# Kernel tuning notes

Hardware: AMD Instinct MI355X
Metric: run time of the kernel (lower is better)

Reference implementation:

```python
import jax, jax.numpy as jnp
import numpy as np

B, T, C, H = 4, 2048, 1024, 16
D = C // H  # head dim = 64


def setup_inputs() -> dict:
    key = jax.random.key(0)
    ks = jax.random.split(key, 5)
    s = 1.0 / np.sqrt(C)
    return {
        "x": jax.random.normal(ks[0], (B, T, C), jnp.float32),
        "Wq": jax.random.normal(ks[1], (C, C), jnp.float32) * s,
        "bq": jnp.zeros((C,), jnp.float32),
        "Wk": jax.random.normal(ks[2], (C, C), jnp.float32) * s,
        "bk": jnp.zeros((C,), jnp.float32),
        "Wv": jax.random.normal(ks[3], (C, C), jnp.float32) * s,
        "bv": jnp.zeros((C,), jnp.float32),
        "Wp": jax.random.normal(ks[4], (C, C), jnp.float32) * s,
        "bp": jnp.zeros((C,), jnp.float32),
    }


def reference(x, Wq, bq, Wk, bk, Wv, bv, Wp, bp):
    # linear projections -> [B, H, T, D]
    def heads(t):
        return t.reshape(B, T, H, D).transpose(0, 2, 1, 3)
    q = heads(x @ Wq.T + bq)
    k = heads(x @ Wk.T + bk)
    v = heads(x @ Wv.T + bv)
    scale = 1.0 / np.sqrt(D)
    att = jnp.einsum("bhtd,bhsd->bhts", q, k) * scale  # [B,H,T,T]
    causal = jnp.tril(jnp.ones((T, T), bool))
    att = jnp.where(causal[None, None], att, -jnp.inf)
    att = jax.nn.softmax(att, axis=-1)
    y = jnp.einsum("bhts,bhsd->bhtd", att, v)  # [B,H,T,D]
    y = y.transpose(0, 2, 1, 3).reshape(B, T, C)
    return y @ Wp.T + bp
```

## Files before the change

### kernel.cpp

```cpp
#include <hip/hip_runtime.h>

typedef float f32x4 __attribute__((ext_vector_type(4)));
typedef float f32x16 __attribute__((ext_vector_type(16)));
typedef __bf16 bf16x8 __attribute__((ext_vector_type(8)));
typedef unsigned short u16x8 __attribute__((ext_vector_type(8)));

#define SCQ 0.1803368801111183f

__device__ inline unsigned short f2bf(float f) {
  unsigned int u = __builtin_bit_cast(unsigned int, f);
  u += 0x7FFFu + ((u >> 16) & 1u);
  return (unsigned short)(u >> 16);
}
__device__ inline unsigned short f2bf_fast(float f) {
  unsigned int u = __builtin_bit_cast(unsigned int, f);
  return (unsigned short)((u + 0x8000u) >> 16);
}

__device__ inline float fexp2(float x) {
#if __has_builtin(__builtin_amdgcn_exp2f)
  return __builtin_amdgcn_exp2f(x);
#else
  return exp2f(x);
#endif
}

template <int N>
__device__ inline float rowror(float v) {
  return __builtin_bit_cast(float, __builtin_amdgcn_update_dpp(
      0, __builtin_bit_cast(int, v), 0x120 | N, 0xF, 0xF, true));
}
__device__ inline float rowsum16(float v) {
  v += rowror<8>(v); v += rowror<4>(v);
  v += rowror<2>(v); v += rowror<1>(v);
  return v;
}

__device__ inline void gload_lds16(const unsigned short* g, unsigned short* l) {
  __builtin_amdgcn_global_load_lds(
      (const __attribute__((address_space(1))) unsigned int*)g,
      (__attribute__((address_space(3))) unsigned int*)l, 16, 0, 0);
}

__global__ void cvt_x(const float* __restrict__ in, unsigned short* __restrict__ out) {
  int i = (blockIdx.x * 256 + threadIdx.x) * 4;
  float4 f = *(const float4*)(in + i);
  ushort4 o;
  o.x = f2bf(f.x); o.y = f2bf(f.y); o.z = f2bf(f.z); o.w = f2bf(f.w);
  *(ushort4*)(out + i) = o;
}

__global__ void cvt_w(const float* __restrict__ a, const float* __restrict__ b,
                      const float* __restrict__ c, const float* __restrict__ d,
                      unsigned short* __restrict__ oa, unsigned short* __restrict__ ob,
                      unsigned short* __restrict__ oc, unsigned short* __restrict__ od) {
  const float* src[4] = {a, b, c, d};
  unsigned short* dst[4] = {oa, ob, oc, od};
  int m = blockIdx.y;
  int i = (blockIdx.x * 256 + threadIdx.x) * 4;
  float4 f = *(const float4*)(src[m] + i);
  ushort4 o;
  o.x = f2bf(f.x); o.y = f2bf(f.y); o.z = f2bf(f.z); o.w = f2bf(f.w);
  *(ushort4*)(dst[m] + i) = o;
}

template <int MODE>
__global__ __launch_bounds__(256) void gemm128(const unsigned short* __restrict__ A,
                                               const unsigned short* __restrict__ Bt,
                                               const float* __restrict__ b0,
                                               const float* __restrict__ b1,
                                               const float* __restrict__ b2,
                                               void* __restrict__ out,
                                               int M, int N, int K) {
  __shared__ __align__(16) unsigned short As[128 * 64];
  __shared__ __align__(16) unsigned short Bs[128 * 64];
  const int tid = threadIdx.x;
  const int lane = tid & 63, w = tid >> 6;
  const int l31 = lane & 31, half = lane >> 5;
  const int wm = w & 1, wn = w >> 1;
  const int m0 = blockIdx.x * 128, n0 = blockIdx.y * 128;

  f32x16 acc[2][2] = {};

  for (int kb = 0; kb < K; kb += 64) {
#pragma unroll
    for (int j = 0; j < 4; j++) {
      int ch = j * 256 + w * 64 + lane;
      int row = ch >> 3, pc = ch & 7;
      int c = pc ^ (row & 7);
      gload_lds16(A + (size_t)(m0 + row) * K + kb + c * 8, As + (size_t)(j * 256 + w * 64) * 8);
      gload_lds16(Bt + (size_t)(n0 + row) * K + kb + c * 8, Bs + (size_t)(j * 256 + w * 64) * 8);
    }
    __syncthreads();
#pragma unroll
    for (int ks = 0; ks < 64; ks += 16) {
      bf16x8 af[2], bfr[2];
#pragma unroll
      for (int at = 0; at < 2; at++) {
        int row = wm * 64 + at * 32 + l31;
        int pc = ((ks >> 3) + half) ^ (row & 7);
        af[at] = *(const bf16x8*)(As + row * 64 + pc * 8);
      }
#pragma unroll
      for (int nt = 0; nt < 2; nt++) {
        int row = wn * 64 + nt * 32 + l31;
        int pc = ((ks >> 3) + half) ^ (row & 7);
        bfr[nt] = *(const bf16x8*)(Bs + row * 64 + pc * 8);
      }
#pragma unroll
      for (int at = 0; at < 2; at++)
#pragma unroll
        for (int nt = 0; nt < 2; nt++)
          acc[at][nt] = __builtin_amdgcn_mfma_f32_32x32x16_bf16(af[at], bfr[nt], acc[at][nt], 0, 0, 0);
    }
    __syncthreads();
  }

#pragma unroll
  for (int at = 0; at < 2; at++)
#pragma unroll
    for (int nt = 0; nt < 2; nt++) {
      int col = n0 + wn * 64 + nt * 32 + l31;
      float bv, sc;
      int which = 0, cl = col;
      if (MODE == 0) {
        which = col >> 10; cl = col & 1023;
        const float* bp = (which == 0) ? b0 : ((which == 1) ? b1 : b2);
        bv = bp[cl];
        sc = (which == 0) ? SCQ : 1.f;
      } else {
        bv = b0[col]; sc = 1.f;
      }
#pragma unroll
      for (int reg = 0; reg < 16; reg++) {
        int row = m0 + wm * 64 + at * 32 + (reg & 3) + 8 * (reg >> 2) + 4 * half;
        float v = (acc[at][nt][reg] + bv) * sc;
        if (MODE == 0) {
          int h = cl >> 6, d = cl & 63;
          int b = row >> 11, t = row & 2047;
          ((unsigned short*)out)[(size_t)which * 8388608 +
                                 ((size_t)((b * 16 + h) * 2048 + t)) * 64 + d] = f2bf(v);
        } else {
          ((float*)out)[(size_t)row * N + col] = v;
        }
      }
    }
}

__global__ __launch_bounds__(256) void transpose_v(const unsigned short* __restrict__ V,
                                                   unsigned short* __restrict__ Vt) {
  constexpr int P = 66;
  __shared__ unsigned short L[64 * P];
  const int tid = threadIdx.x;
  const int bh = blockIdx.y;
  const int t0 = blockIdx.x * 64;
  const unsigned short* Vp = V + (size_t)bh * 2048 * 64;
  unsigned short* Op = Vt + (size_t)bh * 64 * 2048;
#pragma unroll
  for (int j = 0; j < 2; j++) {
    int r = (tid >> 3) + j * 32;
    int c = (tid & 7) * 8;
    u16x8 v = *(const u16x8*)(Vp + (size_t)(t0 + r) * 64 + c);
#pragma unroll
    for (int i = 0; i < 4; i++) {
      unsigned int pk = (unsigned int)v[2 * i] | ((unsigned int)v[2 * i + 1] << 16);
      *(unsigned int*)&L[r * P + c + 2 * i] = pk;
    }
  }
  __syncthreads();
#pragma unroll
  for (int j = 0; j < 2; j++) {
    int ch = j * 256 + tid;
    int d = ch >> 3, tc = (ch & 7) * 8;
    u16x8 o;
#pragma unroll
    for (int k = 0; k < 8; k++) o[k] = L[(tc + k) * P + d];
    *(u16x8*)(Op + (size_t)d * 2048 + t0 + tc) = o;
  }
}

#define PPITCH 72
__device__ __attribute__((always_inline)) inline
void attn_tile(int qt, int s0, const bf16x8* aq, const unsigned short* Ks,
               const unsigned short* Vs, unsigned short* pl,
               f32x4* o, float* lrow, int quad, int l15) {
  const bool full = (s0 + 63) <= qt;
  const int nsc = full ? 4 : (((qt + 15 - s0) >> 4) + 1);
  const int nsc2 = (nsc + 1) & ~1;

#pragma unroll
  for (int sc = 0; sc < 4; sc++) {
    if (sc < nsc) {
      f32x4 s = {};
#pragma unroll
      for (int kh = 0; kh < 2; kh++) {
        int kr = sc * 16 + l15;
        int pc = (kh * 4 + quad) ^ (kr & 7);
        u16x8 bku = *(const u16x8*)(Ks + kr * 64 + pc * 8);
        s = __builtin_amdgcn_mfma_f32_16x16x32_bf16(aq[kh], __builtin_bit_cast(bf16x8, bku), s, 0, 0, 0);
      }
      if (full) {
#pragma unroll
        for (int r = 0; r < 4; r++) {
          float e = fexp2(s[r]);
          lrow[r] += e;
          pl[(quad * 4 + r) * PPITCH + sc * 16 + l15] = f2bf_fast(e);
        }
      } else {
        int sg = s0 + sc * 16 + l15;
#pragma unroll
        for (int r = 0; r < 4; r++) {
          float e = fexp2(s[r]);
          e = (sg > qt + quad * 4 + r) ? 0.f : e;
          lrow[r] += e;
          pl[(quad * 4 + r) * PPITCH + sc * 16 + l15] = f2bf_fast(e);
        }
      }
    } else if (sc < nsc2) {
#pragma unroll
      for (int r = 0; r < 4; r++)
        pl[(quad * 4 + r) * PPITCH + sc * 16 + l15] = 0;
    }
  }
  __asm__ __volatile__("" ::: "memory");
#pragma unroll
  for (int h2 = 0; h2 < 2; h2++) {
    if (h2 * 2 < nsc2) {
      u16x8 apu = *(const u16x8*)(pl + l15 * PPITCH + h2 * 32 + quad * 8);
      bf16x8 ap = __builtin_bit_cast(bf16x8, apu);
#pragma unroll
      for (int dc = 0; dc < 4; dc++) {
        int vr = dc * 16 + l15;
        int pc = (h2 * 4 + quad) ^ (vr & 7);
        u16x8 vu = *(const u16x8*)(Vs + vr * 64 + pc * 8);
        o[dc] = __builtin_amdgcn_mfma_f32_16x16x32_bf16(ap, __builtin_bit_cast(bf16x8, vu), o[dc], 0, 0, 0);
      }
    }
  }
}

__global__ __launch_bounds__(256, 2) void attn_kernel(const unsigned short* __restrict__ Q,
                                                      const unsigned short* __restrict__ Km,
                                                      const unsigned short* __restrict__ Vt,
                                                      unsigned short* __restrict__ Y) {
  constexpr int T = 2048, D = 64;
  __shared__ __align__(16) unsigned short Ks[2][64 * 64];
  __shared__ __align__(16) unsigned short Vs[2][64 * 64];
  __shared__ __align__(16) unsigned short P_lds[4][16 * PPITCH];
  const int tid = threadIdx.x;
  const int lane = tid & 63, w = tid >> 6;
  const int quad = lane >> 4, l15 = lane & 15;
  const int bh = blockIdx.y;
  const int b = bh >> 4, h = bh & 15;
  const int p = blockIdx.x;
  const unsigned short* Qp = Q + (size_t)bh * T * D;
  const unsigned short* Kp = Km + (size_t)bh * T * D;
  const unsigned short* Vp = Vt + (size_t)bh * D * T;
  unsigned short* pl = P_lds[w];

  const int bch0 = (w * 2) * 64, bch1 = (w * 2 + 1) * 64;
  const int ch0 = bch0 + lane, ch1 = bch1 + lane;
  const int row0 = ch0 >> 3, c0 = (ch0 & 7) ^ (row0 & 7);
  const int row1 = ch1 >> 3, c1 = (ch1 & 7) ^ (row1 & 7);

  for (int phase = 0; phase < 2; ++phase) {
    int jlo, jhi;
    if (!phase) { jlo = 8 * p + w; jhi = jlo + 4; }
    else        { jhi = 127 - 8 * p - w; jlo = jhi - 4; }
    const int qlo = jlo * 16, qhi = jhi * 16;
    const int nit = phase ? (32 - 2 * p) : (2 * p + 2);

    bf16x8 aqlo[2], aqhi[2];
    aqlo[0] = *(const bf16x8*)(Qp + (size_t)(qlo + l15) * D + quad * 8);
    aqlo[1] = *(const bf16x8*)(Qp + (size_t)(qlo + l15) * D + 32 + quad * 8);
    aqhi[0] = *(const bf16x8*)(Qp + (size_t)(qhi + l15) * D + quad * 8);
    aqhi[1] = *(const bf16x8*)(Qp + (size_t)(qhi + l15) * D + 32 + quad * 8);

    f32x4 olo[4] = {}, ohi[4] = {};
    float llo[4] = {0.f, 0.f, 0.f, 0.f}, lhi[4] = {0.f, 0.f, 0.f, 0.f};

    gload_lds16(Kp + (size_t)row0 * 64 + c0 * 8, Ks[0] + (size_t)bch0 * 8);
    gload_lds16(Kp + (size_t)row1 * 64 + c1 * 8, Ks[0] + (size_t)bch1 * 8);
    gload_lds16(Vp + (size_t)row0 * T + c0 * 8, Vs[0] + (size_t)bch0 * 8);
    gload_lds16(Vp + (size_t)row1 * T + c1 * 8, Vs[0] + (size_t)bch1 * 8);
    __syncthreads();

    for (int it = 0; it < nit; ++it) {
      const int s0 = it * 64;
      const int cur = it & 1, nxt = cur ^ 1;
      if (it + 1 < nit) {
        const int sn = s0 + 64;
        gload_lds16(Kp + (size_t)(sn + row0) * 64 + c0 * 8, Ks[nxt] + (size_t)bch0 * 8);
        gload_lds16(Kp + (size_t)(sn + row1) * 64 + c1 * 8, Ks[nxt] + (size_t)bch1 * 8);
        gload_lds16(Vp + (size_t)row0 * T + sn + c0 * 8, Vs[nxt] + (size_t)bch0 * 8);
        gload_lds16(Vp + (size_t)row1 * T + sn + c1 * 8, Vs[nxt] + (size_t)bch1 * 8);
      }
      if (s0 <= qlo + 15)
        attn_tile(qlo, s0, aqlo, Ks[cur], Vs[cur], pl, olo, llo, quad, l15);
      attn_tile(qhi, s0, aqhi, Ks[cur], Vs[cur], pl, ohi, lhi, quad, l15);
      __syncthreads();
    }

#pragma unroll
    for (int r = 0; r < 4; r++) {
      float ilo = 1.f / rowsum16(llo[r]);
      float ihi = 1.f / rowsum16(lhi[r]);
      int glo = qlo + quad * 4 + r, ghi = qhi + quad * 4 + r;
#pragma unroll
      for (int dc = 0; dc < 4; dc++) {
        Y[((size_t)(b * T + glo)) * 1024 + h * 64 + dc * 16 + l15] = f2bf(olo[dc][r] * ilo);
        Y[((size_t)(b * T + ghi)) * 1024 + h * 64 + dc * 16 + l15] = f2bf(ohi[dc][r] * ihi);
      }
    }
  }
}

extern "C" void kernel_launch(void* const* d_in, const int* in_sizes, int n_in,
                              void* d_out, int out_size, void* d_ws, size_t ws_size,
                              hipStream_t stream) {
  const float* x  = (const float*)d_in[0];
  const float* Wq = (const float*)d_in[1];
  const float* bq = (const float*)d_in[2];
  const float* Wk = (const float*)d_in[3];
  const float* bk = (const float*)d_in[4];
  const float* Wv = (const float*)d_in[5];
  const float* bv = (const float*)d_in[6];
  const float* Wp = (const float*)d_in[7];
  const float* bp = (const float*)d_in[8];

  char* ws = (char*)d_ws;
  unsigned short* xb  = (unsigned short*)(ws + 0);
  unsigned short* wqb = (unsigned short*)(ws + 16777216);
  unsigned short* wkb = (unsigned short*)(ws + 18874368);
  unsigned short* wvb = (unsigned short*)(ws + 20971520);
  unsigned short* wpb = (unsigned short*)(ws + 23068672);
  unsigned short* Qb  = (unsigned short*)(ws + 25165824);
  unsigned short* Kb  = (unsigned short*)(ws + 41943040);
  unsigned short* Vb  = (unsigned short*)(ws + 58720256);
  unsigned short* Vtb = xb;
  unsigned short* Yb  = Vb;

  cvt_x<<<8192, 256, 0, stream>>>(x, xb);
  cvt_w<<<dim3(1024, 4), 256, 0, stream>>>(Wq, Wk, Wv, Wp, wqb, wkb, wvb, wpb);

  gemm128<0><<<dim3(64, 24), 256, 0, stream>>>(xb, wqb, bq, bk, bv, Qb, 8192, 3072, 1024);

  transpose_v<<<dim3(32, 64), 256, 0, stream>>>(Vb, Vtb);
  attn_kernel<<<dim3(8, 64), 256, 0, stream>>>(Qb, Kb, Vtb, Yb);

  gemm128<1><<<dim3(64, 8), 256, 0, stream>>>(Yb, wpb, bp, bp, bp, d_out, 8192, 1024, 1024);
}
```

Before: 281.3 us.

## Split attention into more smaller blocks with single-buffered K/V and higher occupancy

The attention kernel now gives each wave one 16-row query tile per phase instead of two, and launches 1024 blocks instead of 512, with the grid reordered so consecutive blocks share a query-pair index across heads. K/V double buffering is removed to halve LDS, and launch bounds are raised to four blocks per SM to increase occupancy. Each block reloads K/V per tile and now synchronises twice per iteration with no prefetch overlap. Total K/V traffic also rises, because each K/V tile is now shared by four query tiles instead of eight.

```diff
diff --git a/kernel.cpp b/kernel.cpp
--- a/kernel.cpp
+++ b/kernel.cpp
@@ -239,20 +239,20 @@
   }
 }
 
-__global__ __launch_bounds__(256, 2) void attn_kernel(const unsigned short* __restrict__ Q,
+__global__ __launch_bounds__(256, 4) void attn_kernel(const unsigned short* __restrict__ Q,
                                                       const unsigned short* __restrict__ Km,
                                                       const unsigned short* __restrict__ Vt,
                                                       unsigned short* __restrict__ Y) {
   constexpr int T = 2048, D = 64;
-  __shared__ __align__(16) unsigned short Ks[2][64 * 64];
-  __shared__ __align__(16) unsigned short Vs[2][64 * 64];
+  __shared__ __align__(16) unsigned short Ks[64 * 64];
+  __shared__ __align__(16) unsigned short Vs[64 * 64];
   __shared__ __align__(16) unsigned short P_lds[4][16 * PPITCH];
   const int tid = threadIdx.x;
   const int lane = tid & 63, w = tid >> 6;
   const int quad = lane >> 4, l15 = lane & 15;
-  const int bh = blockIdx.y;
+  const int bh = blockIdx.x;
   const int b = bh >> 4, h = bh & 15;
-  const int p = blockIdx.x;
+  const int p = blockIdx.y;
   const unsigned short* Qp = Q + (size_t)bh * T * D;
   const unsigned short* Kp = Km + (size_t)bh * T * D;
   const unsigned short* Vp = Vt + (size_t)bh * D * T;
@@ -264,53 +264,37 @@
   const int row1 = ch1 >> 3, c1 = (ch1 & 7) ^ (row1 & 7);
 
   for (int phase = 0; phase < 2; ++phase) {
-    int jlo, jhi;
-    if (!phase) { jlo = 8 * p + w; jhi = jlo + 4; }
-    else        { jhi = 127 - 8 * p - w; jlo = jhi - 4; }
-    const int qlo = jlo * 16, qhi = jhi * 16;
-    const int nit = phase ? (32 - 2 * p) : (2 * p + 2);
-
-    bf16x8 aqlo[2], aqhi[2];
-    aqlo[0] = *(const bf16x8*)(Qp + (size_t)(qlo + l15) * D + quad * 8);
-    aqlo[1] = *(const bf16x8*)(Qp + (size_t)(qlo + l15) * D + 32 + quad * 8);
-    aqhi[0] = *(const bf16x8*)(Qp + (size_t)(qhi + l15) * D + quad * 8);
-    aqhi[1] = *(const bf16x8*)(Qp + (size_t)(qhi + l15) * D + 32 + quad * 8);
-
-    f32x4 olo[4] = {}, ohi[4] = {};
-    float llo[4] = {0.f, 0.f, 0.f, 0.f}, lhi[4] = {0.f, 0.f, 0.f, 0.f};
-
-    gload_lds16(Kp + (size_t)row0 * 64 + c0 * 8, Ks[0] + (size_t)bch0 * 8);
-    gload_lds16(Kp + (size_t)row1 * 64 + c1 * 8, Ks[0] + (size_t)bch1 * 8);
-    gload_lds16(Vp + (size_t)row0 * T + c0 * 8, Vs[0] + (size_t)bch0 * 8);
-    gload_lds16(Vp + (size_t)row1 * T + c1 * 8, Vs[0] + (size_t)bch1 * 8);
-    __syncthreads();
+    const int jt = phase ? (127 - (p * 4 + w)) : (p * 4 + w);
+    const int qt = jt * 16;
+    const int nit = phase ? (32 - p) : (p + 1);
+
+    bf16x8 aq[2];
+    aq[0] = *(const bf16x8*)(Qp + (size_t)(qt + l15) * D + quad * 8);
+    aq[1] = *(const bf16x8*)(Qp + (size_t)(qt + l15) * D + 32 + quad * 8);
+
+    f32x4 o[4] = {};
+    float lrow[4] = {0.f, 0.f, 0.f, 0.f};
 
     for (int it = 0; it < nit; ++it) {
       const int s0 = it * 64;
-      const int cur = it & 1, nxt = cur ^ 1;
-      if (it + 1 < nit) {
-        const int sn = s0 + 64;
-        gload_lds16(Kp + (size_t)(sn + row0) * 64 + c0 * 8, Ks[nxt] + (size_t)bch0 * 8);
-        gload_lds16(Kp + (size_t)(sn + row1) * 64 + c1 * 8, Ks[nxt] + (size_t)bch1 * 8);
-        gload_lds16(Vp + (size_t)row0 * T + sn + c0 * 8, Vs[nxt] + (size_t)bch0 * 8);
-        gload_lds16(Vp + (size_t)row1 * T + sn + c1 * 8, Vs[nxt] + (size_t)bch1 * 8);
-      }
-      if (s0 <= qlo + 15)
-        attn_tile(qlo, s0, aqlo, Ks[cur], Vs[cur], pl, olo, llo, quad, l15);
-      attn_tile(qhi, s0, aqhi, Ks[cur], Vs[cur], pl, ohi, lhi, quad, l15);
+      gload_lds16(Kp + (size_t)(s0 + row0) * 64 + c0 * 8, Ks + (size_t)bch0 * 8);
+      gload_lds16(Kp + (size_t)(s0 + row1) * 64 + c1 * 8, Ks + (size_t)bch1 * 8);
+      gload_lds16(Vp + (size_t)row0 * T + s0 + c0 * 8, Vs + (size_t)bch0 * 8);
+      gload_lds16(Vp + (size_t)row1 * T + s0 + c1 * 8, Vs + (size_t)bch1 * 8);
       __syncthreads();
+
+      attn_tile(qt, s0, aq, Ks, Vs, pl, o, lrow, quad, l15);
+
+      __syncthreads();
     }
 
 #pragma unroll
     for (int r = 0; r < 4; r++) {
-      float ilo = 1.f / rowsum16(llo[r]);
-      float ihi = 1.f / rowsum16(lhi[r]);
-      int glo = qlo + quad * 4 + r, ghi = qhi + quad * 4 + r;
-#pragma unroll
-      for (int dc = 0; dc < 4; dc++) {
-        Y[((size_t)(b * T + glo)) * 1024 + h * 64 + dc * 16 + l15] = f2bf(olo[dc][r] * ilo);
-        Y[((size_t)(b * T + ghi)) * 1024 + h * 64 + dc * 16 + l15] = f2bf(ohi[dc][r] * ihi);
-      }
+      float inv = 1.f / rowsum16(lrow[r]);
+      int qg = qt + quad * 4 + r;
+#pragma unroll
+      for (int dc = 0; dc < 4; dc++)
+        Y[((size_t)(b * T + qg)) * 1024 + h * 64 + dc * 16 + l15] = f2bf(o[dc][r] * inv);
     }
   }
 }
@@ -346,7 +330,7 @@
   gemm128<0><<<dim3(64, 24), 256, 0, stream>>>(xb, wqb, bq, bk, bv, Qb, 8192, 3072, 1024);
 
   transpose_v<<<dim3(32, 64), 256, 0, stream>>>(Vb, Vtb);
-  attn_kernel<<<dim3(8, 64), 256, 0, stream>>>(Qb, Kb, Vtb, Yb);
+  attn_kernel<<<dim3(64, 16), 256, 0, stream>>>(Qb, Kb, Vtb, Yb);
 
   gemm128<1><<<dim3(64, 8), 256, 0, stream>>>(Yb, wpb, bp, bp, bp, d_out, 8192, 1024, 1024);
 }
```

Measured after the change: 257.5 us. 8.5% less time.
